# Optimization experiments

Measured on AMD Instinct MI355X. Metric: run time of the kernel, lower is better.

## Reference

```python
import jax, jax.numpy as jnp
import numpy as np

H = 512
A = 16
L = 3
B = 256
T = 512


def layer_norm(x, g, b, eps=1e-5):
    mu = jnp.mean(x, axis=-1, keepdims=True)
    var = jnp.mean((x - mu) ** 2, axis=-1, keepdims=True)
    return (x - mu) * jax.lax.rsqrt(var + eps) * g + b


def setup_inputs() -> dict:
    key = jax.random.key(0)
    ks = jax.random.split(key, 16)
    s = 1.0 / np.sqrt(H)  # keep linear outputs O(1), mimicking orthogonal init scale
    return {
        "hidden": jnp.zeros((B, H), jnp.float32),
        "obs": jax.random.normal(ks[0], (B, T, H), jnp.float32),
        "dones": jax.random.bernoulli(ks[1], 0.01, (B, T)),
        "avail_actions": jnp.ones((B, T, A), jnp.float32),
        "in_w": jax.random.normal(ks[2], (L, H, H), jnp.float32) * s,
        "in_b": jnp.zeros((L, H), jnp.float32),
        "ln_g": jnp.ones((L, H), jnp.float32),
        "ln_b": jnp.zeros((L, H), jnp.float32),
        "gru_wih": jax.random.normal(ks[3], (3 * H, H), jnp.float32) * s,
        "gru_whh": jax.random.normal(ks[4], (3 * H, H), jnp.float32) * s,
        "gru_bih": jnp.zeros((3 * H,), jnp.float32),
        "gru_bhh": jnp.zeros((3 * H,), jnp.float32),
        "am1_w": jax.random.normal(ks[5], (H, H), jnp.float32) * s,
        "am1_b": jnp.zeros((H,), jnp.float32),
        "amln_g": jnp.ones((H,), jnp.float32),
        "amln_b": jnp.zeros((H,), jnp.float32),
        "am2_w": jax.random.normal(ks[6], (A, H), jnp.float32) * s * 0.01,
        "am2_b": jnp.zeros((A,), jnp.float32),
    }


def reference(hidden, obs, dones, avail_actions, in_w, in_b, ln_g, ln_b,
              gru_wih, gru_whh, gru_bih, gru_bhh,
              am1_w, am1_b, amln_g, amln_b, am2_w, am2_b):
    # --- pre-RNN MLP: Linear -> LayerNorm -> ReLU, x3 ---
    emb = obs  # [B,T,H]
    for l in range(L):
        emb = jax.nn.relu(layer_norm(emb @ in_w[l].T + in_b[l], ln_g[l], ln_b[l]))

    # --- GRU scan with reset masking (torch GRUCell math) ---
    def step(h, xt):
        x, r = xt  # x: [B,H], r: [B] bool
        h = jnp.where(r[:, None], 0.0, h)
        gi = x @ gru_wih.T + gru_bih  # [B,3H]
        gh = h @ gru_whh.T + gru_bhh
        i_r, i_z, i_n = jnp.split(gi, 3, axis=-1)
        h_r, h_z, h_n = jnp.split(gh, 3, axis=-1)
        rg = jax.nn.sigmoid(i_r + h_r)
        z = jax.nn.sigmoid(i_z + h_z)
        n = jnp.tanh(i_n + rg * h_n)
        h_new = (1.0 - z) * n + z * h
        return h_new, h_new

    h_final, outs = jax.lax.scan(
        step, hidden, (jnp.swapaxes(emb, 0, 1), dones.T))  # outs: [T,B,H]
    outs = jnp.swapaxes(outs, 0, 1)  # [B,T,H]

    # --- actor head ---
    am = jax.nn.relu(layer_norm(outs @ am1_w.T + am1_b, amln_g, amln_b))
    logits = am @ am2_w.T + am2_b  # [B,T,A]
    logits = logits - (1.0 - avail_actions) * 1e10
    return (h_final, logits)
```

## Files before the change

### kernel.cpp

```cpp
#include <hip/hip_runtime.h>

#define HD 512
#define AD 16
#define BD 256
#define TD 512

using short8  = __attribute__((ext_vector_type(8))) short;
using float4v = __attribute__((ext_vector_type(4))) float;
using ushort4v = __attribute__((ext_vector_type(4))) unsigned short;
typedef unsigned short u16;
typedef unsigned long long u64;

__device__ __forceinline__ u16 f2bf(float f) {
  union { float f; unsigned u; } v; v.f = f;
  unsigned r = v.u + 0x7fffu + ((v.u >> 16) & 1u);
  return (u16)(r >> 16);
}
__device__ __forceinline__ float bf2f(u16 u) {
  union { unsigned u; float f; } c; c.u = ((unsigned)u) << 16; return c.f;
}
__device__ __forceinline__ float fsigm(float x) {
  return __builtin_amdgcn_rcpf(1.f + __builtin_amdgcn_exp2f(-1.4426950408889634f * x));
}
__device__ __forceinline__ float ftanh(float x) {
  float e = __builtin_amdgcn_exp2f(2.8853900817779268f * x);
  return 1.f - 2.f * __builtin_amdgcn_rcpf(1.f + e);
}

__global__ __launch_bounds__(256) void cvt_bf16(const float* __restrict__ in,
                                                u16* __restrict__ out, int n) {
  int i = blockIdx.x * 256 + threadIdx.x;
  int stride = gridDim.x * 256;
  for (; i < n; i += stride) out[i] = f2bf(in[i]);
}

template <bool AF32>
__global__ __launch_bounds__(256) void gemm_ln_relu(
    const void* __restrict__ Ap, const u16* __restrict__ W,
    const float* __restrict__ bias, const float* __restrict__ gam,
    const float* __restrict__ bet, u16* __restrict__ Y) {
  const int r0 = blockIdx.x * 64;
  const int tid = threadIdx.x;
  const int wave = tid >> 6, lane = tid & 63;
  const int lq = lane >> 4, ln16 = lane & 15;

  __shared__ u16 As[64 * 40];
  __shared__ u16 Bs[512 * 40];
  __shared__ float partial[64][4][2];
  __shared__ float murs[64][2];

  float4v acc[4][8];
#pragma unroll
  for (int i = 0; i < 4; ++i)
#pragma unroll
    for (int j = 0; j < 8; ++j) acc[i][j] = (float4v){0.f, 0.f, 0.f, 0.f};

  for (int kk = 0; kk < 16; ++kk) {
    __syncthreads();
    if (AF32) {
      const float* Af = (const float*)Ap;
#pragma unroll
      for (int it = 0; it < 2; ++it) {
        int q = tid + it * 256;
        int row = q >> 3, ko = (q & 7) * 4;
        float4v v = *(const float4v*)(Af + (r0 + row) * 512 + kk * 32 + ko);
        ushort4v o;
        o[0] = f2bf(v[0]); o[1] = f2bf(v[1]); o[2] = f2bf(v[2]); o[3] = f2bf(v[3]);
        *(ushort4v*)(&As[row * 40 + ko]) = o;
      }
    } else {
      const u16* Ab = (const u16*)Ap;
      int row = tid >> 2, ko = (tid & 3) * 8;
      *(short8*)(&As[row * 40 + ko]) =
          *(const short8*)(Ab + (r0 + row) * 512 + kk * 32 + ko);
    }
#pragma unroll
    for (int it = 0; it < 8; ++it) {
      int q = tid + it * 256;
      int row = q >> 2, ko = (q & 3) * 8;
      *(short8*)(&Bs[row * 40 + ko]) =
          *(const short8*)(W + row * 512 + kk * 32 + ko);
    }
    __syncthreads();
    short8 afr[4];
#pragma unroll
    for (int mt = 0; mt < 4; ++mt)
      afr[mt] = *(const short8*)(&As[(mt * 16 + ln16) * 40 + lq * 8]);
#pragma unroll
    for (int nt = 0; nt < 8; ++nt) {
      short8 bfr = *(const short8*)(&Bs[(wave * 128 + nt * 16 + ln16) * 40 + lq * 8]);
#pragma unroll
      for (int mt = 0; mt < 4; ++mt)
        acc[mt][nt] = __builtin_amdgcn_mfma_f32_16x16x32_bf16(afr[mt], bfr, acc[mt][nt], 0, 0, 0);
    }
  }

  float gv[8], bv[8], av[8];
#pragma unroll
  for (int nt = 0; nt < 8; ++nt) {
    int c = wave * 128 + nt * 16 + ln16;
    gv[nt] = gam[c]; bv[nt] = bet[c]; av[nt] = bias[c];
  }
#pragma unroll
  for (int mt = 0; mt < 4; ++mt)
#pragma unroll
    for (int nt = 0; nt < 8; ++nt)
#pragma unroll
      for (int r = 0; r < 4; ++r) acc[mt][nt][r] += av[nt];

#pragma unroll
  for (int mt = 0; mt < 4; ++mt) {
#pragma unroll
    for (int r = 0; r < 4; ++r) {
      float s = 0.f, ss = 0.f;
#pragma unroll
      for (int nt = 0; nt < 8; ++nt) { float v = acc[mt][nt][r]; s += v; ss += v * v; }
#pragma unroll
      for (int off = 1; off < 16; off <<= 1) { s += __shfl_xor(s, off); ss += __shfl_xor(ss, off); }
      if (ln16 == 0) {
        int m = mt * 16 + lq * 4 + r;
        partial[m][wave][0] = s; partial[m][wave][1] = ss;
      }
    }
  }
  __syncthreads();
  if (tid < 64) {
    float s = partial[tid][0][0] + partial[tid][1][0] + partial[tid][2][0] + partial[tid][3][0];
    float ss = partial[tid][0][1] + partial[tid][1][1] + partial[tid][2][1] + partial[tid][3][1];
    float mu = s * (1.f / 512.f);
    float var = ss * (1.f / 512.f) - mu * mu;
    murs[tid][0] = mu;
    murs[tid][1] = rsqrtf(var + 1e-5f);
  }
  __syncthreads();
#pragma unroll
  for (int mt = 0; mt < 4; ++mt) {
#pragma unroll
    for (int r = 0; r < 4; ++r) {
      int m = mt * 16 + lq * 4 + r;
      float mu = murs[m][0], rs = murs[m][1];
#pragma unroll
      for (int nt = 0; nt < 8; ++nt) {
        int c = wave * 128 + nt * 16 + ln16;
        float v = (acc[mt][nt][r] - mu) * rs * gv[nt] + bv[nt];
        Y[(r0 + m) * 512 + c] = f2bf(fmaxf(v, 0.f));
      }
    }
  }
}

__global__ __launch_bounds__(256, 1) void gru_scan(
    const u16* __restrict__ emb, const u16* __restrict__ wih,
    const u16* __restrict__ whh, const float* __restrict__ bih,
    const float* __restrict__ bhh, const float* __restrict__ hidden,
    const int* __restrict__ dones, float* __restrict__ outs,
    float* __restrict__ hfin, u64* __restrict__ hpk, int* __restrict__ flg) {
  const int bg = blockIdx.x >> 5;
  const int cg = blockIdx.x & 31;
  const int c0 = cg * 16;
  const int b0 = bg * 32;
  const int tid = threadIdx.x;
  const int wave = tid >> 6, lane = tid & 63;
  const int lq = lane >> 4, ln16 = lane & 15;

  __shared__ float scr[2][2][3][16][18];
  u16* hpk16 = (u16*)hpk;

  if (wave < 2) {
    const int mt = wave;
    const int rowA = b0 + mt * 16 + ln16;

    short8 wr_[48];
#pragma unroll
    for (int g = 0; g < 3; ++g)
#pragma unroll
      for (int kk = 0; kk < 16; ++kk)
        wr_[g * 16 + kk] =
            *(const short8*)(whh + (g * 512 + c0 + ln16) * 512 + kk * 32 + lq * 8);

    float bi[3], bhv[3];
#pragma unroll
    for (int g = 0; g < 3; ++g) {
      bi[g]  = bih[g * 512 + c0 + ln16];
      bhv[g] = bhh[g * 512 + c0 + ln16];
    }
    float hprev[4];
#pragma unroll
    for (int r = 0; r < 4; ++r)
      hprev[r] = hidden[(b0 + mt * 16 + lq * 4 + r) * 512 + c0 + ln16];

    int* myslot = flg + ((bg * 2 + mt) * 32 + cg) * 16;
    const int* pollp = flg + ((bg * 2 + mt) * 32 + (lane & 31)) * 16;

    __syncthreads();

    for (int t = 0; t < TD; ++t) {
      int dnr[4];
#pragma unroll
      for (int r = 0; r < 4; ++r)
        dnr[r] = dones[(b0 + mt * 16 + lq * 4 + r) * 512 + t];
      float giv[3][4];
#pragma unroll
      for (int g = 0; g < 3; ++g)
#pragma unroll
        for (int r = 0; r < 4; ++r) giv[g][r] = scr[t & 1][mt][g][lq * 4 + r][ln16];

      if (t > 0) {
        int guard = 0;
        for (;;) {
          int v = __hip_atomic_load(pollp, __ATOMIC_RELAXED, __HIP_MEMORY_SCOPE_AGENT);
          if (__all(v >= t)) break;
          if (++guard > (1 << 18)) break;
        }
      }

      u64 av[32];
      if (t == 0) {
#pragma unroll
        for (int kk = 0; kk < 16; ++kk) {
          const float* hp = hidden + rowA * 512 + lq * 8 + kk * 32;
          float4v h0 = *(const float4v*)(hp);
          float4v h1 = *(const float4v*)(hp + 4);
          av[2 * kk] = (u64)f2bf(h0[0]) | ((u64)f2bf(h0[1]) << 16) |
                       ((u64)f2bf(h0[2]) << 32) | ((u64)f2bf(h0[3]) << 48);
          av[2 * kk + 1] = (u64)f2bf(h1[0]) | ((u64)f2bf(h1[1]) << 16) |
                           ((u64)f2bf(h1[2]) << 32) | ((u64)f2bf(h1[3]) << 48);
        }
      } else {
        u64* hb = hpk + ((t - 1) & 1) * 32768 + rowA * 128 + lq * 2;
#pragma unroll
        for (int kk = 0; kk < 16; ++kk) {
          av[2 * kk]     = __hip_atomic_load(hb + kk * 8,     __ATOMIC_RELAXED, __HIP_MEMORY_SCOPE_AGENT);
          av[2 * kk + 1] = __hip_atomic_load(hb + kk * 8 + 1, __ATOMIC_RELAXED, __HIP_MEMORY_SCOPE_AGENT);
        }
      }

      float4v agh[3];
#pragma unroll
      for (int g = 0; g < 3; ++g) agh[g] = (float4v){0.f, 0.f, 0.f, 0.f};
#pragma unroll
      for (int kk = 0; kk < 16; ++kk) {
        union { u64 q[2]; short8 v; } u;
        u.q[0] = av[2 * kk]; u.q[1] = av[2 * kk + 1];
#pragma unroll
        for (int g = 0; g < 3; ++g)
          agh[g] = __builtin_amdgcn_mfma_f32_16x16x32_bf16(u.v, wr_[g * 16 + kk], agh[g], 0, 0, 0);
      }

      float hv[4];
#pragma unroll
      for (int r = 0; r < 4; ++r) {
        bool d = dnr[r] != 0;
        float h  = d ? 0.f : hprev[r];
        float g0 = d ? 0.f : agh[0][r];
        float g1 = d ? 0.f : agh[1][r];
        float g2 = d ? 0.f : agh[2][r];
        float rg = fsigm(giv[0][r] + bi[0] + g0 + bhv[0]);
        float z  = fsigm(giv[1][r] + bi[1] + g1 + bhv[1]);
        float nn = ftanh(giv[2][r] + bi[2] + rg * (g2 + bhv[2]));
        hv[r] = (1.f - z) * nn + z * h;
        hprev[r] = hv[r];
      }

#pragma unroll
      for (int r = 0; r < 4; ++r) {
        int b = b0 + mt * 16 + lq * 4 + r;
        __hip_atomic_store(hpk16 + (t & 1) * 131072 + b * 512 + c0 + ln16,
                           f2bf(hv[r]), __ATOMIC_RELAXED, __HIP_MEMORY_SCOPE_AGENT);
      }
      asm volatile("s_waitcnt vmcnt(0)" ::: "memory");
      if (lane == 0 && t < TD - 1)
        __hip_atomic_store(myslot, t + 1, __ATOMIC_RELAXED, __HIP_MEMORY_SCOPE_AGENT);

#pragma unroll
      for (int r = 0; r < 4; ++r) {
        int b = b0 + mt * 16 + lq * 4 + r;
        outs[(t * 256 + b) * 512 + c0 + ln16] = hv[r];
        if (t == TD - 1) hfin[b * 512 + c0 + ln16] = hv[r];
      }
      __syncthreads();
    }
  } else {
    const int mt = wave - 2;

    short8 wf[48];
#pragma unroll
    for (int g = 0; g < 3; ++g)
#pragma unroll
      for (int kk = 0; kk < 16; ++kk)
        wf[g * 16 + kk] =
            *(const short8*)(wih + (g * 512 + c0 + ln16) * 512 + kk * 32 + lq * 8);

    const int row = b0 + mt * 16 + ln16;
    auto produce = [&](int tp) {
      const u16* ap = emb + (row * 512 + tp) * 512 + lq * 8;
      float4v acc[3];
#pragma unroll
      for (int g = 0; g < 3; ++g) acc[g] = (float4v){0.f, 0.f, 0.f, 0.f};
#pragma unroll
      for (int kk = 0; kk < 16; ++kk) {
        short8 af = *(const short8*)(ap + kk * 32);
#pragma unroll
        for (int g = 0; g < 3; ++g)
          acc[g] = __builtin_amdgcn_mfma_f32_16x16x32_bf16(af, wf[g * 16 + kk], acc[g], 0, 0, 0);
      }
#pragma unroll
      for (int g = 0; g < 3; ++g)
#pragma unroll
        for (int r = 0; r < 4; ++r)
          scr[tp & 1][mt][g][lq * 4 + r][ln16] = acc[g][r];
    };

    produce(0);
    __syncthreads();

    for (int t = 0; t < TD; ++t) {
      if (t + 1 < TD) produce(t + 1);
      __syncthreads();
    }
  }
}

__global__ __launch_bounds__(256) void head_logits(
    const u16* __restrict__ am, const float* __restrict__ w2,
    const float* __restrict__ b2, const float* __restrict__ avail,
    float* __restrict__ out) {
  int r = blockIdx.x * 16 + (threadIdx.x >> 4);
  int a = threadIdx.x & 15;
  int t = r >> 8, b = r & 255;
  const u16* ar = am + r * 512;
  const float* wr = w2 + a * 512;
  float acc = 0.f;
  for (int k = 0; k < 512; k += 8) {
    short8 v = *(const short8*)(ar + k);
    float4v w0 = *(const float4v*)(wr + k);
    float4v w1 = *(const float4v*)(wr + k + 4);
    acc += bf2f((u16)v[0]) * w0[0] + bf2f((u16)v[1]) * w0[1] +
           bf2f((u16)v[2]) * w0[2] + bf2f((u16)v[3]) * w0[3] +
           bf2f((u16)v[4]) * w1[0] + bf2f((u16)v[5]) * w1[1] +
           bf2f((u16)v[6]) * w1[2] + bf2f((u16)v[7]) * w1[3];
  }
  int oi = (b * 512 + t) * 16 + a;
  float avv = avail[oi];
  out[oi] = acc + b2[a] - (1.f - avv) * 1e10f;
}

extern "C" void kernel_launch(void* const* d_in, const int* in_sizes, int n_in,
                              void* d_out, int out_size, void* d_ws, size_t ws_size,
                              hipStream_t stream) {
  (void)in_sizes; (void)n_in; (void)out_size; (void)ws_size;
  const float* hidden = (const float*)d_in[0];
  const float* obs    = (const float*)d_in[1];
  const int*   dones  = (const int*)d_in[2];
  const float* avail  = (const float*)d_in[3];
  const float* in_w   = (const float*)d_in[4];
  const float* in_b   = (const float*)d_in[5];
  const float* ln_g   = (const float*)d_in[6];
  const float* ln_b   = (const float*)d_in[7];
  const float* gwih   = (const float*)d_in[8];
  const float* gwhh   = (const float*)d_in[9];
  const float* gbih   = (const float*)d_in[10];
  const float* gbhh   = (const float*)d_in[11];
  const float* am1w   = (const float*)d_in[12];
  const float* am1b   = (const float*)d_in[13];
  const float* amg    = (const float*)d_in[14];
  const float* amb    = (const float*)d_in[15];
  const float* am2w   = (const float*)d_in[16];
  const float* am2b   = (const float*)d_in[17];

  char* ws = (char*)d_ws;
  u16*   embA  = (u16*)(ws);
  u16*   embB  = (u16*)(ws + 134217728);
  float* outs  = (float*)(ws + 268435456);
  u16*   w_in  = (u16*)(ws + 536870912);
  u16*   w_ih  = w_in + 786432;
  u16*   w_hh  = w_ih + 786432;
  u16*   w_a1  = w_hh + 786432;
  int*   flg   = (int*)(ws + 536870912 + 5242880);
  u64*   hpk   = (u64*)(ws + 536870912 + 5242880 + 32768);

  hipMemsetAsync(flg, 0, 32768, stream);
  cvt_bf16<<<1024, 256, 0, stream>>>(in_w, w_in, 786432);
  cvt_bf16<<<1024, 256, 0, stream>>>(gwih, w_ih, 786432);
  cvt_bf16<<<1024, 256, 0, stream>>>(gwhh, w_hh, 786432);
  cvt_bf16<<<512, 256, 0, stream>>>(am1w, w_a1, 262144);

  gemm_ln_relu<true ><<<2048, 256, 0, stream>>>(obs,  w_in,          in_b,        ln_g,        ln_b,        embA);
  gemm_ln_relu<false><<<2048, 256, 0, stream>>>(embA, w_in + 262144, in_b + 512,  ln_g + 512,  ln_b + 512,  embB);
  gemm_ln_relu<false><<<2048, 256, 0, stream>>>(embB, w_in + 524288, in_b + 1024, ln_g + 1024, ln_b + 1024, embA);

  gru_scan<<<256, 256, 0, stream>>>(embA, w_ih, w_hh, gbih, gbhh, hidden, dones,
                                    outs, (float*)d_out, hpk, flg);

  gemm_ln_relu<true ><<<2048, 256, 0, stream>>>(outs, w_a1, am1b, amg, amb, embB);
  head_logits<<<8192, 256, 0, stream>>>(embB, am2w, am2b, avail, (float*)d_out + 131072);
}
```

Baseline: 4.645 ms.

## Replace block barriers with per-wave LDS flags and use cache-bypassing hidden loads

Removes the per-step __syncthreads between the recurrent waves and the input-projection producer waves. They now hand off through shared-memory counters (pf/ec), so producers can run up to two steps ahead in the double buffer and the pairs of waves are decoupled. Hidden-state exchange loads switch from per-u64 atomic loads to inline-asm dwordx4 loads with sc0 sc1 cache bits, the flag stride shrinks, and s_sleep is added to the cross-block poll. This risks ordering bugs if the LDS flag handshakes are wrong, and the spin timeout is shortened.

```diff
diff --git a/kernel.cpp b/kernel.cpp
--- a/kernel.cpp
+++ b/kernel.cpp
@@ -164,7 +164,12 @@
   const int lq = lane >> 4, ln16 = lane & 15;
 
   __shared__ float scr[2][2][3][16][18];
+  __shared__ int pf[2];
+  __shared__ int ec[2];
   u16* hpk16 = (u16*)hpk;
+
+  if (tid == 0) { pf[0] = 0; pf[1] = 0; ec[0] = 0; ec[1] = 0; }
+  __syncthreads();
 
   if (wave < 2) {
     const int mt = wave;
@@ -189,63 +194,70 @@
     for (int r = 0; r < 4; ++r)
       hprev[r] = hidden[(b0 + mt * 16 + lq * 4 + r) * 512 + c0 + ln16];
 
-    int* myslot = flg + ((bg * 2 + mt) * 32 + cg) * 16;
-    const int* pollp = flg + ((bg * 2 + mt) * 32 + (lane & 31)) * 16;
-
-    __syncthreads();
+    int* myslot = flg + ((bg * 2 + mt) * 32 + cg) * 4;
+    const int* pollp = flg + ((bg * 2 + mt) * 32 + (lane & 31)) * 4;
 
     for (int t = 0; t < TD; ++t) {
+      {
+        int guard = 0;
+        while (__hip_atomic_load(&pf[mt], __ATOMIC_RELAXED, __HIP_MEMORY_SCOPE_WORKGROUP) < t + 1) {
+          if (++guard > (1 << 18)) break;
+        }
+      }
+      float giv[3][4];
+#pragma unroll
+      for (int g = 0; g < 3; ++g)
+#pragma unroll
+        for (int r = 0; r < 4; ++r) giv[g][r] = scr[t & 1][mt][g][lq * 4 + r][ln16];
+      asm volatile("s_waitcnt lgkmcnt(0)" ::: "memory");
+      if (lane == 0)
+        __hip_atomic_store(&ec[mt], t + 1, __ATOMIC_RELAXED, __HIP_MEMORY_SCOPE_WORKGROUP);
+
       int dnr[4];
 #pragma unroll
       for (int r = 0; r < 4; ++r)
         dnr[r] = dones[(b0 + mt * 16 + lq * 4 + r) * 512 + t];
-      float giv[3][4];
-#pragma unroll
-      for (int g = 0; g < 3; ++g)
-#pragma unroll
-        for (int r = 0; r < 4; ++r) giv[g][r] = scr[t & 1][mt][g][lq * 4 + r][ln16];
 
       if (t > 0) {
         int guard = 0;
         for (;;) {
           int v = __hip_atomic_load(pollp, __ATOMIC_RELAXED, __HIP_MEMORY_SCOPE_AGENT);
           if (__all(v >= t)) break;
-          if (++guard > (1 << 18)) break;
+          if (++guard > (1 << 16)) break;
+          __builtin_amdgcn_s_sleep(2);
         }
       }
 
-      u64 av[32];
+      short8 hfr[16];
       if (t == 0) {
 #pragma unroll
         for (int kk = 0; kk < 16; ++kk) {
           const float* hp = hidden + rowA * 512 + lq * 8 + kk * 32;
           float4v h0 = *(const float4v*)(hp);
           float4v h1 = *(const float4v*)(hp + 4);
-          av[2 * kk] = (u64)f2bf(h0[0]) | ((u64)f2bf(h0[1]) << 16) |
-                       ((u64)f2bf(h0[2]) << 32) | ((u64)f2bf(h0[3]) << 48);
-          av[2 * kk + 1] = (u64)f2bf(h1[0]) | ((u64)f2bf(h1[1]) << 16) |
-                           ((u64)f2bf(h1[2]) << 32) | ((u64)f2bf(h1[3]) << 48);
+          union { u16 s[8]; short8 v; } u;
+          u.s[0] = f2bf(h0[0]); u.s[1] = f2bf(h0[1]); u.s[2] = f2bf(h0[2]); u.s[3] = f2bf(h0[3]);
+          u.s[4] = f2bf(h1[0]); u.s[5] = f2bf(h1[1]); u.s[6] = f2bf(h1[2]); u.s[7] = f2bf(h1[3]);
+          hfr[kk] = u.v;
         }
       } else {
-        u64* hb = hpk + ((t - 1) & 1) * 32768 + rowA * 128 + lq * 2;
-#pragma unroll
-        for (int kk = 0; kk < 16; ++kk) {
-          av[2 * kk]     = __hip_atomic_load(hb + kk * 8,     __ATOMIC_RELAXED, __HIP_MEMORY_SCOPE_AGENT);
-          av[2 * kk + 1] = __hip_atomic_load(hb + kk * 8 + 1, __ATOMIC_RELAXED, __HIP_MEMORY_SCOPE_AGENT);
-        }
+        const char* hb = (const char*)hpk + ((t - 1) & 1) * 262144 + rowA * 1024 + lq * 16;
+#pragma unroll
+        for (int kk = 0; kk < 16; ++kk)
+          asm volatile("global_load_dwordx4 %0, %1, off offset:%c2 sc0 sc1"
+                       : "=v"(hfr[kk]) : "v"(hb), "i"(kk * 64));
+        asm volatile("s_waitcnt vmcnt(0)" ::: "memory");
+        __builtin_amdgcn_sched_barrier(0);
       }
 
       float4v agh[3];
 #pragma unroll
       for (int g = 0; g < 3; ++g) agh[g] = (float4v){0.f, 0.f, 0.f, 0.f};
 #pragma unroll
-      for (int kk = 0; kk < 16; ++kk) {
-        union { u64 q[2]; short8 v; } u;
-        u.q[0] = av[2 * kk]; u.q[1] = av[2 * kk + 1];
+      for (int kk = 0; kk < 16; ++kk)
 #pragma unroll
         for (int g = 0; g < 3; ++g)
-          agh[g] = __builtin_amdgcn_mfma_f32_16x16x32_bf16(u.v, wr_[g * 16 + kk], agh[g], 0, 0, 0);
-      }
+          agh[g] = __builtin_amdgcn_mfma_f32_16x16x32_bf16(hfr[kk], wr_[g * 16 + kk], agh[g], 0, 0, 0);
 
       float hv[4];
 #pragma unroll
@@ -278,7 +290,6 @@
         outs[(t * 256 + b) * 512 + c0 + ln16] = hv[r];
         if (t == TD - 1) hfin[b * 512 + c0 + ln16] = hv[r];
       }
-      __syncthreads();
     }
   } else {
     const int mt = wave - 2;
@@ -309,14 +320,19 @@
 #pragma unroll
         for (int r = 0; r < 4; ++r)
           scr[tp & 1][mt][g][lq * 4 + r][ln16] = acc[g][r];
+      asm volatile("s_waitcnt lgkmcnt(0)" ::: "memory");
+      if (lane == 0)
+        __hip_atomic_store(&pf[mt], tp + 1, __ATOMIC_RELAXED, __HIP_MEMORY_SCOPE_WORKGROUP);
     };
 
     produce(0);
-    __syncthreads();
-
-    for (int t = 0; t < TD; ++t) {
-      if (t + 1 < TD) produce(t + 1);
-      __syncthreads();
+    produce(1);
+    for (int tp = 2; tp < TD; ++tp) {
+      int guard = 0;
+      while (__hip_atomic_load(&ec[mt], __ATOMIC_RELAXED, __HIP_MEMORY_SCOPE_WORKGROUP) < tp - 1) {
+        if (++guard > (1 << 18)) break;
+      }
+      produce(tp);
     }
   }
 }
```

After: 4.223 ms. 9.1% less time.
